# Kernel optimization log

Measured on AMD Instinct MI355X. Metric: run time of the kernel, lower is better.

## Reference

```python
import jax, jax.numpy as jnp
import numpy as np
from jax import lax

# dims (match init_kwargs)
NC, BS, H, W, OC, NT = 4, 16, 64, 64, 12, 32


def _conv(x, w):
    # NHWC 'same' 3x3 conv
    return lax.conv_general_dilated(x, w, (1, 1), 'SAME',
                                    dimension_numbers=('NHWC', 'HWIO', 'NHWC'))


def _convlstm_step(x, h, c, Wx, Wh, b):
    # Keras ConvLSTM2D, single timestep. Gate order i, f, g(c), o; activation=tanh,
    # recurrent_activation=hard_sigmoid.
    z = _conv(x, Wx) + _conv(h, Wh) + b
    i, f, g, o = jnp.split(z, 4, axis=-1)
    i = jax.nn.hard_sigmoid(i)
    f = jax.nn.hard_sigmoid(f)
    o = jax.nn.hard_sigmoid(o)
    c_new = f * c + i * jnp.tanh(g)
    h_new = o * jnp.tanh(c_new)
    return h_new, c_new


def setup_inputs() -> dict:
    key = jax.random.key(0)
    ks = jax.random.split(key, 8)
    sc = lambda k, shp: jax.random.normal(k, shp, jnp.float32) * 0.05
    return {
        'x': jax.random.normal(ks[0], (BS, NT, H, W, OC), jnp.float32),
        'class_ids': jax.random.randint(ks[1], (NT,), 0, NC),
        'Wx_g': sc(ks[2], (3, 3, NC * OC, 4 * OC)),  # general cell input kernel
        'Wh_g': sc(ks[3], (3, 3, OC, 4 * OC)),       # general cell recurrent kernel
        'b_g': jnp.zeros((4 * OC,), jnp.float32),
        'Wx_c': sc(ks[4], (3, 3, 2 * OC, 4 * OC)),   # class cell input kernel
        'Wh_c': sc(ks[5], (3, 3, OC, 4 * OC)),       # class cell recurrent kernel
        'b_c': jnp.zeros((4 * OC,), jnp.float32),
    }


def reference(x, class_ids, Wx_g, Wh_g, b_g, Wx_c, Wh_c, b_c):
    def step(carry, inp):
        class_h, class_c, gen_h, gen_c = carry
        frame, cid = inp
        # general cell reads the whole class-state bank (raw reshape, as in TF source)
        x_gen = jnp.reshape(class_h, (BS, H, W, NC * OC))
        gen_h, gen_c = _convlstm_step(x_gen, gen_h, gen_c, Wx_g, Wh_g, b_g)
        # class cell reads frame + fresh general representation
        aug = jnp.concatenate([frame, gen_h], axis=-1)  # (BS,H,W,2*OC)
        h_new, c_new = _convlstm_step(aug, class_h[cid], class_c[cid], Wx_c, Wh_c, b_c)
        # scatter update into class-indexed state banks
        class_h = class_h.at[cid].set(h_new)
        class_c = class_c.at[cid].set(c_new)
        return (class_h, class_c, gen_h, gen_c), h_new.reshape(BS, -1)

    z = jnp.zeros((NC, BS, H, W, OC), jnp.float32)
    g = jnp.zeros((BS, H, W, OC), jnp.float32)
    xs = (jnp.swapaxes(x, 0, 1), class_ids)  # time-major
    _, outs = lax.scan(step, (z, z, g, g), xs)
    # OuterLayer: sum over time of flattened per-step outputs
    return jnp.sum(outs, axis=0)  # (BS, H*W*OC)
```

## Files before the change

### kernel.cpp

```cpp
#include <hip/hip_runtime.h>
#include <hip/hip_bf16.h>

#define NCLS 4
#define BS   16
#define NT   32
#define OC   12
#define HW   4096
#define PIX  65536
#define STATE 786432
#define BANK  3145728

typedef short bf16x8 __attribute__((ext_vector_type(8)));
typedef float f32x4  __attribute__((ext_vector_type(4)));

__device__ __forceinline__ float hsig(float v){
    return fminf(fmaxf((v + 3.0f) * (1.0f/6.0f), 0.0f), 1.0f);
}
__device__ __forceinline__ short f2bf(float f){
    union { __hip_bfloat16 h; short s; } u;
    u.h = __float2bfloat16(f);
    return u.s;
}

__global__ __launch_bounds__(256) void repack_kernel(
    const float* __restrict__ Wxg, const float* __restrict__ Whg,
    const float* __restrict__ Wxc, const float* __restrict__ Whc,
    bf16x8* __restrict__ wgt)
{
    int id = blockIdx.x * 256 + threadIdx.x;
    if (id >= 6912) return;
    int cell = id / 3456;
    int rem  = id - cell * 3456;
    int tap  = rem / 384;  rem -= tap * 384;
    int kb   = rem / 192;  rem -= kb * 192;
    int nt   = rem / 64;
    int lane = rem - nt * 64;
    int quad = lane >> 4;
    int n    = nt * 16 + (lane & 15);
    union { bf16x8 v; short s[8]; } o;
    #pragma unroll
    for (int j = 0; j < 8; ++j){
        int k = kb * 32 + quad * 8 + j;
        float f = 0.0f;
        if (cell == 0){
            if (k < 48)      f = Wxg[(tap*48 + k)*48 + n];
            else if (k < 60) f = Whg[(tap*12 + (k-48))*48 + n];
        } else {
            if (k < 24)      f = Wxc[(tap*24 + k)*48 + n];
            else if (k < 36) f = Whc[(tap*12 + (k-24))*48 + n];
        }
        o.s[j] = f2bf(f);
    }
    wgt[id] = o.v;
}

#define HALO_SHORTS (4*198*8)

__device__ __forceinline__ int row_swizzle(int bid){
    return ((bid & 7) << 7) | (bid >> 3);
}

__global__ __launch_bounds__(256, 4) void gen_kernel(
    short* __restrict__ bank,
    const short* __restrict__ hin,
    short* __restrict__ hout,
    float* __restrict__ cstate,
    const short* __restrict__ htmp_prev,
    const int* __restrict__ ids, int t,
    const bf16x8* __restrict__ wgt,
    const float* __restrict__ bias)
{
    __shared__ __align__(16) short halo[HALO_SHORTS];
    const int tid = threadIdx.x;
    const int rb  = row_swizzle(blockIdx.x);
    const int p0  = rb << 6;
    const int b   = p0 >> 12;
    const int y   = (p0 >> 6) & 63;

    const int cprev = (t > 0) ? ids[t-1] : -1;
    const bool slotmatch = (cprev >= 0) && ((b >> 2) == cprev);
    const short* bsrc = slotmatch ? htmp_prev : bank;

    const int i = tid;
    const bool active = (i < 198);
    {
        int r  = i / 66, c = i - r * 66;
        int yy = y + r - 1, xx = c - 1;
        bool valid = active & (yy >= 0) & (yy < 64) & (xx >= 0) & (xx < 64);
        int p  = (b << 12) + (yy << 6) + xx;
        int pb = slotmatch ? (p & 16383) : p;
        uint4 bk[6]; uint2 h0, h1, h2;
        #pragma unroll
        for (int q = 0; q < 6; ++q) bk[q] = make_uint4(0u,0u,0u,0u);
        h0 = make_uint2(0u,0u); h1 = h0; h2 = h0;
        if (valid){
            const short* bp = bsrc + pb*48;
            #pragma unroll
            for (int q = 0; q < 6; ++q) bk[q] = *(const uint4*)(bp + q*8);
            h0 = *(const uint2*)(hin + p*12);
            h1 = *(const uint2*)(hin + p*12 + 4);
            h2 = *(const uint2*)(hin + p*12 + 8);
            if (slotmatch && r == 1){
                #pragma unroll
                for (int q = 0; q < 6; ++q)
                    *(uint4*)(bank + p*48 + q*8) = bk[q];
            }
        }
        if (active){
            #pragma unroll
            for (int q = 0; q < 4; ++q)
                *(uint4*)&halo[(q*198 + i)*8] = bk[q];
        }
        __syncthreads();

        const int lane = tid & 63;
        const int w    = tid >> 6;
        const int m    = lane & 15;
        const int quad = lane >> 4;
        const int colbase = 16*w + m;

        f32x4 acc0 = {0.f,0.f,0.f,0.f};
        f32x4 acc1 = acc0, acc2 = acc0;

        #pragma unroll
        for (int ky = 0; ky < 3; ++ky){
            #pragma unroll
            for (int kx = 0; kx < 3; ++kx){
                const int tap = ky*3 + kx;
                const bf16x8 a = *(const bf16x8*)
                    &halo[((quad*198) + ky*66 + colbase + kx)*8];
                const bf16x8* wp = wgt + ((tap*2 + 0)*3)*64 + lane;
                acc0 = __builtin_amdgcn_mfma_f32_16x16x32_bf16(a, wp[0],   acc0, 0,0,0);
                acc1 = __builtin_amdgcn_mfma_f32_16x16x32_bf16(a, wp[64],  acc1, 0,0,0);
                acc2 = __builtin_amdgcn_mfma_f32_16x16x32_bf16(a, wp[128], acc2, 0,0,0);
            }
        }
        __syncthreads();

        if (active){
            *(uint4*)&halo[(0*198 + i)*8] = bk[4];
            *(uint4*)&halo[(1*198 + i)*8] = bk[5];
            union { uint2 u2[2]; uint4 u4; } p2, p3;
            p2.u2[0] = h0; p2.u2[1] = h1;
            p3.u2[0] = h2; p3.u2[1] = make_uint2(0u,0u);
            *(uint4*)&halo[(2*198 + i)*8] = p2.u4;
            *(uint4*)&halo[(3*198 + i)*8] = p3.u4;
        }
        __syncthreads();

        #pragma unroll
        for (int ky = 0; ky < 3; ++ky){
            #pragma unroll
            for (int kx = 0; kx < 3; ++kx){
                const int tap = ky*3 + kx;
                const bf16x8 a = *(const bf16x8*)
                    &halo[((quad*198) + ky*66 + colbase + kx)*8];
                const bf16x8* wp = wgt + ((tap*2 + 1)*3)*64 + lane;
                acc0 = __builtin_amdgcn_mfma_f32_16x16x32_bf16(a, wp[0],   acc0, 0,0,0);
                acc1 = __builtin_amdgcn_mfma_f32_16x16x32_bf16(a, wp[64],  acc1, 0,0,0);
                acc2 = __builtin_amdgcn_mfma_f32_16x16x32_bf16(a, wp[128], acc2, 0,0,0);
            }
        }
        __syncthreads();

        float* zw = ((float*)halo) + w * 768;
        #pragma unroll
        for (int r2 = 0; r2 < 4; ++r2){
            zw[(quad*4 + r2)*48 +      m] = acc0[r2];
            zw[(quad*4 + r2)*48 + 16 + m] = acc1[r2];
            zw[(quad*4 + r2)*48 + 32 + m] = acc2[r2];
        }
        __syncthreads();
        const int pbase = p0 + 16*w;
        #pragma unroll
        for (int s = 0; s < 3; ++s){
            int idx = lane*3 + s;
            int px  = idx / 12;
            int j   = idx - px*12;
            float zi = zw[px*48 +      j] + bias[j];
            float zf = zw[px*48 + 12 + j] + bias[12 + j];
            float zg = zw[px*48 + 24 + j] + bias[24 + j];
            float zo = zw[px*48 + 36 + j] + bias[36 + j];
            int off = pbase*12 + idx;
            float cold = cstate[off];
            float cn = hsig(zf)*cold + hsig(zi)*tanhf(zg);
            cstate[off] = cn;
            hout[off] = f2bf(hsig(zo)*tanhf(cn));
        }
    }
}

__global__ __launch_bounds__(256, 4) void class_kernel(
    const float* __restrict__ xall,
    const int*   __restrict__ ids, int t,
    const short* __restrict__ ghn,
    const short* __restrict__ bank,
    float* __restrict__ class_c,
    const bf16x8* __restrict__ wgt,
    const float* __restrict__ bias,
    short* __restrict__ htmp,
    float* __restrict__ out)
{
    __shared__ __align__(16) short halo[HALO_SHORTS];
    const int tid = threadIdx.x;
    const int rb  = row_swizzle(blockIdx.x);
    const int p0  = rb << 6;
    const int b   = p0 >> 12;
    const int y   = (p0 >> 6) & 63;
    const int cid = ids[t];
    const short* chs   = bank + (size_t)cid * STATE;
    const float* frame = xall + (size_t)(b*NT + t) * (HW*12);

    const int i = tid;
    const bool active = (i < 198);
    {
        int r  = i / 66, c = i - r * 66;
        int yy = y + r - 1, xx = c - 1;
        bool valid = active & (yy >= 0) & (yy < 64) & (xx >= 0) & (xx < 64);
        int pl = (yy << 6) + xx;
        int p  = (b << 12) + pl;
        float4 f0, f1, f2;
        f0 = make_float4(0.f,0.f,0.f,0.f); f1 = f0; f2 = f0;
        uint2 g0, g1, g2, s0, s1, s2;
        g0 = make_uint2(0u,0u); g1 = g0; g2 = g0; s0 = g0; s1 = g0; s2 = g0;
        if (valid){
            f0 = *(const float4*)(frame + pl*12);
            f1 = *(const float4*)(frame + pl*12 + 4);
            f2 = *(const float4*)(frame + pl*12 + 8);
            g0 = *(const uint2*)(ghn + p*12);
            g1 = *(const uint2*)(ghn + p*12 + 4);
            g2 = *(const uint2*)(ghn + p*12 + 8);
            s0 = *(const uint2*)(chs + p*12);
            s1 = *(const uint2*)(chs + p*12 + 4);
            s2 = *(const uint2*)(chs + p*12 + 8);
        }
        if (active){
            union { uint4 u4; uint2 u2[2]; short s[8]; } pk;
            pk.s[0]=f2bf(f0.x); pk.s[1]=f2bf(f0.y); pk.s[2]=f2bf(f0.z); pk.s[3]=f2bf(f0.w);
            pk.s[4]=f2bf(f1.x); pk.s[5]=f2bf(f1.y); pk.s[6]=f2bf(f1.z); pk.s[7]=f2bf(f1.w);
            *(uint4*)&halo[(0*198 + i)*8] = pk.u4;
            pk.s[0]=f2bf(f2.x); pk.s[1]=f2bf(f2.y); pk.s[2]=f2bf(f2.z); pk.s[3]=f2bf(f2.w);
            pk.u2[1] = g0;
            *(uint4*)&halo[(1*198 + i)*8] = pk.u4;
            pk.u2[0] = g1; pk.u2[1] = g2;
            *(uint4*)&halo[(2*198 + i)*8] = pk.u4;
            pk.u2[0] = s0; pk.u2[1] = s1;
            *(uint4*)&halo[(3*198 + i)*8] = pk.u4;
        }
        __syncthreads();

        const int lane = tid & 63;
        const int w    = tid >> 6;
        const int m    = lane & 15;
        const int quad = lane >> 4;
        const int colbase = 16*w + m;

        f32x4 acc0 = {0.f,0.f,0.f,0.f};
        f32x4 acc1 = acc0, acc2 = acc0;

        #pragma unroll
        for (int ky = 0; ky < 3; ++ky){
            #pragma unroll
            for (int kx = 0; kx < 3; ++kx){
                const int tap = ky*3 + kx;
                const bf16x8 a = *(const bf16x8*)
                    &halo[((quad*198) + ky*66 + colbase + kx)*8];
                const bf16x8* wp = wgt + ((tap*2 + 0)*3)*64 + lane;
                acc0 = __builtin_amdgcn_mfma_f32_16x16x32_bf16(a, wp[0],   acc0, 0,0,0);
                acc1 = __builtin_amdgcn_mfma_f32_16x16x32_bf16(a, wp[64],  acc1, 0,0,0);
                acc2 = __builtin_amdgcn_mfma_f32_16x16x32_bf16(a, wp[128], acc2, 0,0,0);
            }
        }
        __syncthreads();

        if (active){
            union { uint4 u4; uint2 u2[2]; } p0k;
            p0k.u2[0] = s2; p0k.u2[1] = make_uint2(0u,0u);
            uint4 z = make_uint4(0u,0u,0u,0u);
            *(uint4*)&halo[(0*198 + i)*8] = p0k.u4;
            *(uint4*)&halo[(1*198 + i)*8] = z;
            *(uint4*)&halo[(2*198 + i)*8] = z;
            *(uint4*)&halo[(3*198 + i)*8] = z;
        }
        __syncthreads();

        #pragma unroll
        for (int ky = 0; ky < 3; ++ky){
            #pragma unroll
            for (int kx = 0; kx < 3; ++kx){
                const int tap = ky*3 + kx;
                const bf16x8 a = *(const bf16x8*)
                    &halo[((quad*198) + ky*66 + colbase + kx)*8];
                const bf16x8* wp = wgt + ((tap*2 + 1)*3)*64 + lane;
                acc0 = __builtin_amdgcn_mfma_f32_16x16x32_bf16(a, wp[0],   acc0, 0,0,0);
                acc1 = __builtin_amdgcn_mfma_f32_16x16x32_bf16(a, wp[64],  acc1, 0,0,0);
                acc2 = __builtin_amdgcn_mfma_f32_16x16x32_bf16(a, wp[128], acc2, 0,0,0);
            }
        }
        __syncthreads();

        float* zw = ((float*)halo) + w * 768;
        #pragma unroll
        for (int r2 = 0; r2 < 4; ++r2){
            zw[(quad*4 + r2)*48 +      m] = acc0[r2];
            zw[(quad*4 + r2)*48 + 16 + m] = acc1[r2];
            zw[(quad*4 + r2)*48 + 32 + m] = acc2[r2];
        }
        __syncthreads();
        float* cc = class_c + (size_t)cid * STATE;
        const int pbase = p0 + 16*w;
        #pragma unroll
        for (int s = 0; s < 3; ++s){
            int idx = lane*3 + s;
            int px  = idx / 12;
            int j   = idx - px*12;
            float zi = zw[px*48 +      j] + bias[j];
            float zf = zw[px*48 + 12 + j] + bias[12 + j];
            float zg = zw[px*48 + 24 + j] + bias[24 + j];
            float zo = zw[px*48 + 36 + j] + bias[36 + j];
            int off = pbase*12 + idx;
            float cold = cc[off];
            float cn = hsig(zf)*cold + hsig(zi)*tanhf(zg);
            cc[off] = cn;
            float h = hsig(zo)*tanhf(cn);
            htmp[off] = f2bf(h);
            out[off] += h;
        }
    }
}

extern "C" void kernel_launch(void* const* d_in, const int* in_sizes, int n_in,
                              void* d_out, int out_size, void* d_ws, size_t ws_size,
                              hipStream_t stream)
{
    (void)in_sizes; (void)n_in; (void)out_size; (void)ws_size;
    const float* x    = (const float*)d_in[0];
    const int*   ids  = (const int*)  d_in[1];
    const float* Wxg  = (const float*)d_in[2];
    const float* Whg  = (const float*)d_in[3];
    const float* bg   = (const float*)d_in[4];
    const float* Wxc  = (const float*)d_in[5];
    const float* Whc  = (const float*)d_in[6];
    const float* bc   = (const float*)d_in[7];
    float* out = (float*)d_out;

    char* base = (char*)d_ws;
    short*  bank    = (short*) (base);
    float*  class_c = (float*) (base + 6291456);
    short*  genh0   = (short*) (base + 18874368);
    short*  genh1   = (short*) (base + 20447232);
    float*  gen_c   = (float*) (base + 22020096);
    short*  htmp0   = (short*) (base + 25165824);
    short*  htmp1   = (short*) (base + 26738688);
    bf16x8* wgt     = (bf16x8*)(base + 28311552);
    const bf16x8* wgt_gen = wgt;
    const bf16x8* wgt_cls = wgt + 3456;

    hipMemsetAsync(bank,    0, (size_t)2*BANK,  stream);
    hipMemsetAsync(class_c, 0, (size_t)4*BANK,  stream);
    hipMemsetAsync(genh0,   0, (size_t)2*STATE, stream);
    hipMemsetAsync(gen_c,   0, (size_t)4*STATE, stream);
    hipMemsetAsync(out,     0, (size_t)4*STATE, stream);

    repack_kernel<<<27, 256, 0, stream>>>(Wxg, Whg, Wxc, Whc, wgt);

    for (int t = 0; t < NT; ++t){
        short* hin       = (t & 1) ? genh1 : genh0;
        short* hnew      = (t & 1) ? genh0 : genh1;
        short* htmp_prev = (t & 1) ? htmp0 : htmp1;
        short* htmp_new  = (t & 1) ? htmp1 : htmp0;
        gen_kernel<<<1024, 256, 0, stream>>>(bank, hin, hnew, gen_c,
                                             htmp_prev, ids, t, wgt_gen, bg);
        class_kernel<<<1024, 256, 0, stream>>>(x, ids, t, hnew, bank, class_c,
                                               wgt_cls, bc, htmp_new, out);
    }
}
```

Measured before the change: 1.065 ms.

## Fuse general and class ConvLSTM cells into one per-step kernel with halo recompute

Merges the two per-timestep kernels into a single step kernel. Each block recomputes the general cell over three rows (its own row plus neighbours) so the class cell's 3x3 conv can read the fresh general hidden state from shared memory without a grid-wide dependency. This halves the launches and removes a global round-trip of the general hidden state. It also pre-converts x to bf16 once, and double-buffers the general cell state so neighbouring blocks read unmodified values. The cost is about three times the general-cell MFMA work per block, plus more shared memory, and occupancy drops to 2 blocks per CU.

```diff
diff --git a/kernel.cpp b/kernel.cpp
--- a/kernel.cpp
+++ b/kernel.cpp
@@ -12,6 +12,7 @@
 
 typedef short bf16x8 __attribute__((ext_vector_type(8)));
 typedef float f32x4  __attribute__((ext_vector_type(4)));
+typedef unsigned long long u64;
 
 __device__ __forceinline__ float hsig(float v){
     return fminf(fmaxf((v + 3.0f) * (1.0f/6.0f), 0.0f), 1.0f);
@@ -54,279 +55,230 @@
     wgt[id] = o.v;
 }
 
-#define HALO_SHORTS (4*198*8)
+__global__ __launch_bounds__(256) void cvt_kernel(
+    const float* __restrict__ x, short* __restrict__ xbf)
+{
+    for (int i = blockIdx.x*256 + threadIdx.x; i < 6291456; i += 2048*256){
+        float4 f = ((const float4*)x)[i];
+        union { u64 q; short s[4]; } pk;
+        pk.s[0]=f2bf(f.x); pk.s[1]=f2bf(f.y); pk.s[2]=f2bf(f.z); pk.s[3]=f2bf(f.w);
+        ((u64*)xbf)[i] = pk.q;
+    }
+}
+
+#define REC 72
 
 __device__ __forceinline__ int row_swizzle(int bid){
     return ((bid & 7) << 7) | (bid >> 3);
 }
 
-__global__ __launch_bounds__(256, 4) void gen_kernel(
+#define MFMA __builtin_amdgcn_mfma_f32_16x16x32_bf16
+
+__global__ __launch_bounds__(256, 2) void step_kernel(
+    const short* __restrict__ xbf,
+    const int*   __restrict__ ids, int t,
     short* __restrict__ bank,
-    const short* __restrict__ hin,
-    short* __restrict__ hout,
-    float* __restrict__ cstate,
-    const short* __restrict__ htmp_prev,
-    const int* __restrict__ ids, int t,
+    const short* __restrict__ hin,  short* __restrict__ hnew,
+    const short* __restrict__ htp,  short* __restrict__ htn,
+    const float* __restrict__ gcs,  float* __restrict__ gcd,
+    float* __restrict__ class_c,
     const bf16x8* __restrict__ wgt,
-    const float* __restrict__ bias)
+    const float* __restrict__ bias_g, const float* __restrict__ bias_c,
+    float* __restrict__ out)
 {
-    __shared__ __align__(16) short halo[HALO_SHORTS];
+    __shared__ __align__(16) short grec[5*66*REC];
+    __shared__ __align__(16) short crec[3*66*REC];
+    __shared__ __align__(8)  short hrow[768];
+
     const int tid = threadIdx.x;
     const int rb  = row_swizzle(blockIdx.x);
     const int p0  = rb << 6;
     const int b   = p0 >> 12;
     const int y   = (p0 >> 6) & 63;
-
+    const int lane = tid & 63, w = tid >> 6, m = lane & 15, quad = lane >> 4;
+    const int colbase = 16*w + m;
+    const int cid   = ids[t];
     const int cprev = (t > 0) ? ids[t-1] : -1;
     const bool slotmatch = (cprev >= 0) && ((b >> 2) == cprev);
-    const short* bsrc = slotmatch ? htmp_prev : bank;
-
-    const int i = tid;
-    const bool active = (i < 198);
+    const bf16x8* wgt_cls = wgt + 3456;
+    const short* xframe = xbf + (size_t)(b*NT + t)*(HW*12);
+    const short* chs = (cid == cprev) ? htp : (bank + (size_t)cid*STATE);
+
     {
-        int r  = i / 66, c = i - r * 66;
-        int yy = y + r - 1, xx = c - 1;
-        bool valid = active & (yy >= 0) & (yy < 64) & (xx >= 0) & (xx < 64);
-        int p  = (b << 12) + (yy << 6) + xx;
-        int pb = slotmatch ? (p & 16383) : p;
-        uint4 bk[6]; uint2 h0, h1, h2;
-        #pragma unroll
-        for (int q = 0; q < 6; ++q) bk[q] = make_uint4(0u,0u,0u,0u);
-        h0 = make_uint2(0u,0u); h1 = h0; h2 = h0;
-        if (valid){
-            const short* bp = bsrc + pb*48;
+        const uint4 z = make_uint4(0u,0u,0u,0u);
+        uint4* g4 = (uint4*)grec;
+        for (int j = tid; j < 2970; j += 256) g4[j] = z;
+        uint4* c4 = (uint4*)crec;
+        for (int j = tid; j < 1782; j += 256) c4[j] = z;
+    }
+    __syncthreads();
+
+    for (int pos = tid; pos < 330; pos += 256){
+        int r = pos/66, c = pos - r*66;
+        int yy = y + r - 2, xx = c - 1;
+        if (yy >= 0 && yy < 64 && xx >= 0 && xx < 64){
+            int p = (b<<12) + (yy<<6) + xx;
+            const short* src = slotmatch ? (htp + (size_t)(p & 16383)*48)
+                                         : (bank + (size_t)p*48);
+            short* dst = &grec[pos*REC];
+            uint4 v[6];
             #pragma unroll
-            for (int q = 0; q < 6; ++q) bk[q] = *(const uint4*)(bp + q*8);
-            h0 = *(const uint2*)(hin + p*12);
-            h1 = *(const uint2*)(hin + p*12 + 4);
-            h2 = *(const uint2*)(hin + p*12 + 8);
-            if (slotmatch && r == 1){
+            for (int q = 0; q < 6; ++q) v[q] = *(const uint4*)(src + q*8);
+            #pragma unroll
+            for (int q = 0; q < 6; ++q) *(uint4*)(dst + q*8) = v[q];
+            *(u64*)(dst+48) = *(const u64*)(hin + (size_t)p*12);
+            *(u64*)(dst+52) = *(const u64*)(hin + (size_t)p*12 + 4);
+            *(u64*)(dst+56) = *(const u64*)(hin + (size_t)p*12 + 8);
+            if (slotmatch && r == 2){
                 #pragma unroll
                 for (int q = 0; q < 6; ++q)
-                    *(uint4*)(bank + p*48 + q*8) = bk[q];
+                    *(uint4*)(bank + (size_t)p*48 + q*8) = v[q];
             }
         }
-        if (active){
-            #pragma unroll
-            for (int q = 0; q < 4; ++q)
-                *(uint4*)&halo[(q*198 + i)*8] = bk[q];
-        }
-        __syncthreads();
-
-        const int lane = tid & 63;
-        const int w    = tid >> 6;
-        const int m    = lane & 15;
-        const int quad = lane >> 4;
-        const int colbase = 16*w + m;
-
-        f32x4 acc0 = {0.f,0.f,0.f,0.f};
-        f32x4 acc1 = acc0, acc2 = acc0;
-
+    }
+    if (tid < 198){
+        int pos = tid;
+        int r = pos/66, c = pos - r*66;
+        int yy = y + r - 1, xx = c - 1;
+        if (yy >= 0 && yy < 64 && xx >= 0 && xx < 64){
+            int p   = (b<<12) + (yy<<6) + xx;
+            int pim = (yy<<6) + xx;
+            short* dst = &crec[pos*REC];
+            *(u64*)(dst+0)  = *(const u64*)(xframe + (size_t)pim*12);
+            *(u64*)(dst+4)  = *(const u64*)(xframe + (size_t)pim*12 + 4);
+            *(u64*)(dst+8)  = *(const u64*)(xframe + (size_t)pim*12 + 8);
+            *(u64*)(dst+24) = *(const u64*)(chs + (size_t)p*12);
+            *(u64*)(dst+28) = *(const u64*)(chs + (size_t)p*12 + 4);
+            *(u64*)(dst+32) = *(const u64*)(chs + (size_t)p*12 + 8);
+        }
+    }
+    __syncthreads();
+
+    f32x4 ga[3][3];
+    #pragma unroll
+    for (int rr = 0; rr < 3; ++rr){
+        #pragma unroll
+        for (int q = 0; q < 3; ++q){
+            f32x4 zz = {0.f,0.f,0.f,0.f};
+            ga[rr][q] = zz;
+        }
+    }
+    #pragma unroll
+    for (int rr = 0; rr < 3; ++rr){
         #pragma unroll
         for (int ky = 0; ky < 3; ++ky){
             #pragma unroll
             for (int kx = 0; kx < 3; ++kx){
                 const int tap = ky*3 + kx;
-                const bf16x8 a = *(const bf16x8*)
-                    &halo[((quad*198) + ky*66 + colbase + kx)*8];
-                const bf16x8* wp = wgt + ((tap*2 + 0)*3)*64 + lane;
-                acc0 = __builtin_amdgcn_mfma_f32_16x16x32_bf16(a, wp[0],   acc0, 0,0,0);
-                acc1 = __builtin_amdgcn_mfma_f32_16x16x32_bf16(a, wp[64],  acc1, 0,0,0);
-                acc2 = __builtin_amdgcn_mfma_f32_16x16x32_bf16(a, wp[128], acc2, 0,0,0);
+                const int rec = ((rr+ky)*66 + colbase + kx)*REC;
+                const bf16x8 a0 = *(const bf16x8*)&grec[rec + quad*8];
+                const bf16x8 a1 = *(const bf16x8*)&grec[rec + 32 + quad*8];
+                const bf16x8* wp0 = wgt + ((tap*2 + 0)*3)*64 + lane;
+                const bf16x8* wp1 = wgt + ((tap*2 + 1)*3)*64 + lane;
+                ga[rr][0] = MFMA(a0, wp0[0],   ga[rr][0], 0,0,0);
+                ga[rr][1] = MFMA(a0, wp0[64],  ga[rr][1], 0,0,0);
+                ga[rr][2] = MFMA(a0, wp0[128], ga[rr][2], 0,0,0);
+                ga[rr][0] = MFMA(a1, wp1[0],   ga[rr][0], 0,0,0);
+                ga[rr][1] = MFMA(a1, wp1[64],  ga[rr][1], 0,0,0);
+                ga[rr][2] = MFMA(a1, wp1[128], ga[rr][2], 0,0,0);
             }
         }
+    }
+    __syncthreads();
+
+    float* zw = ((float*)grec) + w * 768;
+    #pragma unroll
+    for (int rr = 0; rr < 3; ++rr){
+        int oy = y + rr - 1;
+        if (oy < 0 || oy > 63) continue;
+        #pragma unroll
+        for (int r2 = 0; r2 < 4; ++r2){
+            zw[(quad*4 + r2)*48 +      m] = ga[rr][0][r2];
+            zw[(quad*4 + r2)*48 + 16 + m] = ga[rr][1][r2];
+            zw[(quad*4 + r2)*48 + 32 + m] = ga[rr][2][r2];
+        }
         __syncthreads();
-
-        if (active){
-            *(uint4*)&halo[(0*198 + i)*8] = bk[4];
-            *(uint4*)&halo[(1*198 + i)*8] = bk[5];
-            union { uint2 u2[2]; uint4 u4; } p2, p3;
-            p2.u2[0] = h0; p2.u2[1] = h1;
-            p3.u2[0] = h2; p3.u2[1] = make_uint2(0u,0u);
-            *(uint4*)&halo[(2*198 + i)*8] = p2.u4;
-            *(uint4*)&halo[(3*198 + i)*8] = p3.u4;
-        }
-        __syncthreads();
-
-        #pragma unroll
-        for (int ky = 0; ky < 3; ++ky){
-            #pragma unroll
-            for (int kx = 0; kx < 3; ++kx){
-                const int tap = ky*3 + kx;
-                const bf16x8 a = *(const bf16x8*)
-                    &halo[((quad*198) + ky*66 + colbase + kx)*8];
-                const bf16x8* wp = wgt + ((tap*2 + 1)*3)*64 + lane;
-                acc0 = __builtin_amdgcn_mfma_f32_16x16x32_bf16(a, wp[0],   acc0, 0,0,0);
-                acc1 = __builtin_amdgcn_mfma_f32_16x16x32_bf16(a, wp[64],  acc1, 0,0,0);
-                acc2 = __builtin_amdgcn_mfma_f32_16x16x32_bf16(a, wp[128], acc2, 0,0,0);
-            }
-        }
-        __syncthreads();
-
-        float* zw = ((float*)halo) + w * 768;
-        #pragma unroll
-        for (int r2 = 0; r2 < 4; ++r2){
-            zw[(quad*4 + r2)*48 +      m] = acc0[r2];
-            zw[(quad*4 + r2)*48 + 16 + m] = acc1[r2];
-            zw[(quad*4 + r2)*48 + 32 + m] = acc2[r2];
-        }
-        __syncthreads();
-        const int pbase = p0 + 16*w;
+        const int obase = (b<<12) + (oy<<6) + 16*w;
         #pragma unroll
         for (int s = 0; s < 3; ++s){
             int idx = lane*3 + s;
             int px  = idx / 12;
             int j   = idx - px*12;
-            float zi = zw[px*48 +      j] + bias[j];
-            float zf = zw[px*48 + 12 + j] + bias[12 + j];
-            float zg = zw[px*48 + 24 + j] + bias[24 + j];
-            float zo = zw[px*48 + 36 + j] + bias[36 + j];
-            int off = pbase*12 + idx;
-            float cold = cstate[off];
+            float zi = zw[px*48 +      j] + bias_g[j];
+            float zf = zw[px*48 + 12 + j] + bias_g[12 + j];
+            float zg = zw[px*48 + 24 + j] + bias_g[24 + j];
+            float zo = zw[px*48 + 36 + j] + bias_g[36 + j];
+            int off = obase*12 + idx;
+            float cold = gcs[off];
             float cn = hsig(zf)*cold + hsig(zi)*tanhf(zg);
-            cstate[off] = cn;
-            hout[off] = f2bf(hsig(zo)*tanhf(cn));
-        }
-    }
-}
-
-__global__ __launch_bounds__(256, 4) void class_kernel(
-    const float* __restrict__ xall,
-    const int*   __restrict__ ids, int t,
-    const short* __restrict__ ghn,
-    const short* __restrict__ bank,
-    float* __restrict__ class_c,
-    const bf16x8* __restrict__ wgt,
-    const float* __restrict__ bias,
-    short* __restrict__ htmp,
-    float* __restrict__ out)
-{
-    __shared__ __align__(16) short halo[HALO_SHORTS];
-    const int tid = threadIdx.x;
-    const int rb  = row_swizzle(blockIdx.x);
-    const int p0  = rb << 6;
-    const int b   = p0 >> 12;
-    const int y   = (p0 >> 6) & 63;
-    const int cid = ids[t];
-    const short* chs   = bank + (size_t)cid * STATE;
-    const float* frame = xall + (size_t)(b*NT + t) * (HW*12);
-
-    const int i = tid;
-    const bool active = (i < 198);
+            if (rr == 1) gcd[off] = cn;
+            float h = hsig(zo)*tanhf(cn);
+            crec[(rr*66 + 16*w + px + 1)*REC + 12 + j] = f2bf(h);
+            if (rr == 1) hrow[w*192 + idx] = f2bf(h);
+        }
+        __syncthreads();
+    }
+    __syncthreads();
+
+    if (tid < 192)
+        ((u64*)(hnew + (size_t)p0*12))[tid] = ((const u64*)hrow)[tid];
+
+    f32x4 ca[3];
     {
-        int r  = i / 66, c = i - r * 66;
-        int yy = y + r - 1, xx = c - 1;
-        bool valid = active & (yy >= 0) & (yy < 64) & (xx >= 0) & (xx < 64);
-        int pl = (yy << 6) + xx;
-        int p  = (b << 12) + pl;
-        float4 f0, f1, f2;
-        f0 = make_float4(0.f,0.f,0.f,0.f); f1 = f0; f2 = f0;
-        uint2 g0, g1, g2, s0, s1, s2;
-        g0 = make_uint2(0u,0u); g1 = g0; g2 = g0; s0 = g0; s1 = g0; s2 = g0;
-        if (valid){
-            f0 = *(const float4*)(frame + pl*12);
-            f1 = *(const float4*)(frame + pl*12 + 4);
-            f2 = *(const float4*)(frame + pl*12 + 8);
-            g0 = *(const uint2*)(ghn + p*12);
-            g1 = *(const uint2*)(ghn + p*12 + 4);
-            g2 = *(const uint2*)(ghn + p*12 + 8);
-            s0 = *(const uint2*)(chs + p*12);
-            s1 = *(const uint2*)(chs + p*12 + 4);
-            s2 = *(const uint2*)(chs + p*12 + 8);
-        }
-        if (active){
-            union { uint4 u4; uint2 u2[2]; short s[8]; } pk;
-            pk.s[0]=f2bf(f0.x); pk.s[1]=f2bf(f0.y); pk.s[2]=f2bf(f0.z); pk.s[3]=f2bf(f0.w);
-            pk.s[4]=f2bf(f1.x); pk.s[5]=f2bf(f1.y); pk.s[6]=f2bf(f1.z); pk.s[7]=f2bf(f1.w);
-            *(uint4*)&halo[(0*198 + i)*8] = pk.u4;
-            pk.s[0]=f2bf(f2.x); pk.s[1]=f2bf(f2.y); pk.s[2]=f2bf(f2.z); pk.s[3]=f2bf(f2.w);
-            pk.u2[1] = g0;
-            *(uint4*)&halo[(1*198 + i)*8] = pk.u4;
-            pk.u2[0] = g1; pk.u2[1] = g2;
-            *(uint4*)&halo[(2*198 + i)*8] = pk.u4;
-            pk.u2[0] = s0; pk.u2[1] = s1;
-            *(uint4*)&halo[(3*198 + i)*8] = pk.u4;
-        }
-        __syncthreads();
-
-        const int lane = tid & 63;
-        const int w    = tid >> 6;
-        const int m    = lane & 15;
-        const int quad = lane >> 4;
-        const int colbase = 16*w + m;
-
-        f32x4 acc0 = {0.f,0.f,0.f,0.f};
-        f32x4 acc1 = acc0, acc2 = acc0;
-
-        #pragma unroll
-        for (int ky = 0; ky < 3; ++ky){
-            #pragma unroll
-            for (int kx = 0; kx < 3; ++kx){
-                const int tap = ky*3 + kx;
-                const bf16x8 a = *(const bf16x8*)
-                    &halo[((quad*198) + ky*66 + colbase + kx)*8];
-                const bf16x8* wp = wgt + ((tap*2 + 0)*3)*64 + lane;
-                acc0 = __builtin_amdgcn_mfma_f32_16x16x32_bf16(a, wp[0],   acc0, 0,0,0);
-                acc1 = __builtin_amdgcn_mfma_f32_16x16x32_bf16(a, wp[64],  acc1, 0,0,0);
-                acc2 = __builtin_amdgcn_mfma_f32_16x16x32_bf16(a, wp[128], acc2, 0,0,0);
-            }
-        }
-        __syncthreads();
-
-        if (active){
-            union { uint4 u4; uint2 u2[2]; } p0k;
-            p0k.u2[0] = s2; p0k.u2[1] = make_uint2(0u,0u);
-            uint4 z = make_uint4(0u,0u,0u,0u);
-            *(uint4*)&halo[(0*198 + i)*8] = p0k.u4;
-            *(uint4*)&halo[(1*198 + i)*8] = z;
-            *(uint4*)&halo[(2*198 + i)*8] = z;
-            *(uint4*)&halo[(3*198 + i)*8] = z;
-        }
-        __syncthreads();
-
-        #pragma unroll
-        for (int ky = 0; ky < 3; ++ky){
-            #pragma unroll
-            for (int kx = 0; kx < 3; ++kx){
-                const int tap = ky*3 + kx;
-                const bf16x8 a = *(const bf16x8*)
-                    &halo[((quad*198) + ky*66 + colbase + kx)*8];
-                const bf16x8* wp = wgt + ((tap*2 + 1)*3)*64 + lane;
-                acc0 = __builtin_amdgcn_mfma_f32_16x16x32_bf16(a, wp[0],   acc0, 0,0,0);
-                acc1 = __builtin_amdgcn_mfma_f32_16x16x32_bf16(a, wp[64],  acc1, 0,0,0);
-                acc2 = __builtin_amdgcn_mfma_f32_16x16x32_bf16(a, wp[128], acc2, 0,0,0);
-            }
-        }
-        __syncthreads();
-
-        float* zw = ((float*)halo) + w * 768;
-        #pragma unroll
-        for (int r2 = 0; r2 < 4; ++r2){
-            zw[(quad*4 + r2)*48 +      m] = acc0[r2];
-            zw[(quad*4 + r2)*48 + 16 + m] = acc1[r2];
-            zw[(quad*4 + r2)*48 + 32 + m] = acc2[r2];
-        }
-        __syncthreads();
+        f32x4 zz = {0.f,0.f,0.f,0.f};
+        ca[0] = zz; ca[1] = zz; ca[2] = zz;
+    }
+    #pragma unroll
+    for (int ky = 0; ky < 3; ++ky){
+        #pragma unroll
+        for (int kx = 0; kx < 3; ++kx){
+            const int tap = ky*3 + kx;
+            const int rec = (ky*66 + colbase + kx)*REC;
+            const bf16x8 a0 = *(const bf16x8*)&crec[rec + quad*8];
+            const bf16x8 a1 = *(const bf16x8*)&crec[rec + 32 + quad*8];
+            const bf16x8* wp0 = wgt_cls + ((tap*2 + 0)*3)*64 + lane;
+            const bf16x8* wp1 = wgt_cls + ((tap*2 + 1)*3)*64 + lane;
+            ca[0] = MFMA(a0, wp0[0],   ca[0], 0,0,0);
+            ca[1] = MFMA(a0, wp0[64],  ca[1], 0,0,0);
+            ca[2] = MFMA(a0, wp0[128], ca[2], 0,0,0);
+            ca[0] = MFMA(a1, wp1[0],   ca[0], 0,0,0);
+            ca[1] = MFMA(a1, wp1[64],  ca[1], 0,0,0);
+            ca[2] = MFMA(a1, wp1[128], ca[2], 0,0,0);
+        }
+    }
+    __syncthreads();
+
+    #pragma unroll
+    for (int r2 = 0; r2 < 4; ++r2){
+        zw[(quad*4 + r2)*48 +      m] = ca[0][r2];
+        zw[(quad*4 + r2)*48 + 16 + m] = ca[1][r2];
+        zw[(quad*4 + r2)*48 + 32 + m] = ca[2][r2];
+    }
+    __syncthreads();
+    {
         float* cc = class_c + (size_t)cid * STATE;
-        const int pbase = p0 + 16*w;
+        const int obase = p0 + 16*w;
         #pragma unroll
         for (int s = 0; s < 3; ++s){
             int idx = lane*3 + s;
             int px  = idx / 12;
             int j   = idx - px*12;
-            float zi = zw[px*48 +      j] + bias[j];
-            float zf = zw[px*48 + 12 + j] + bias[12 + j];
-            float zg = zw[px*48 + 24 + j] + bias[24 + j];
-            float zo = zw[px*48 + 36 + j] + bias[36 + j];
-            int off = pbase*12 + idx;
+            float zi = zw[px*48 +      j] + bias_c[j];
+            float zf = zw[px*48 + 12 + j] + bias_c[12 + j];
+            float zg = zw[px*48 + 24 + j] + bias_c[24 + j];
+            float zo = zw[px*48 + 36 + j] + bias_c[36 + j];
+            int off = obase*12 + idx;
             float cold = cc[off];
             float cn = hsig(zf)*cold + hsig(zi)*tanhf(zg);
             cc[off] = cn;
             float h = hsig(zo)*tanhf(cn);
-            htmp[off] = f2bf(h);
             out[off] += h;
-        }
-    }
+            hrow[w*192 + idx] = f2bf(h);
+        }
+    }
+    __syncthreads();
+    if (tid < 192)
+        ((u64*)(htn + (size_t)p0*12))[tid] = ((const u64*)hrow)[tid];
 }
 
 extern "C" void kernel_launch(void* const* d_in, const int* in_sizes, int n_in,
@@ -346,32 +298,35 @@
 
     char* base = (char*)d_ws;
     short*  bank    = (short*) (base);
-    float*  class_c = (float*) (base + 6291456);
-    short*  genh0   = (short*) (base + 18874368);
-    short*  genh1   = (short*) (base + 20447232);
-    float*  gen_c   = (float*) (base + 22020096);
-    short*  htmp0   = (short*) (base + 25165824);
-    short*  htmp1   = (short*) (base + 26738688);
-    bf16x8* wgt     = (bf16x8*)(base + 28311552);
-    const bf16x8* wgt_gen = wgt;
-    const bf16x8* wgt_cls = wgt + 3456;
-
-    hipMemsetAsync(bank,    0, (size_t)2*BANK,  stream);
-    hipMemsetAsync(class_c, 0, (size_t)4*BANK,  stream);
-    hipMemsetAsync(genh0,   0, (size_t)2*STATE, stream);
-    hipMemsetAsync(gen_c,   0, (size_t)4*STATE, stream);
-    hipMemsetAsync(out,     0, (size_t)4*STATE, stream);
+    short*  genh0   = (short*) (base + 6291456);
+    short*  genh1   = (short*) (base + 7864320);
+    short*  htmp0   = (short*) (base + 9437184);
+    short*  htmp1   = (short*) (base + 11010048);
+    float*  gen_cA  = (float*) (base + 12582912);
+    float*  gen_cB  = (float*) (base + 15728640);
+    float*  class_c = (float*) (base + 18874368);
+    bf16x8* wgt     = (bf16x8*)(base + 31457280);
+    short*  xbf     = (short*) (base + 31567872);
+
+    hipMemsetAsync(bank,    0, 6291456,  stream);
+    hipMemsetAsync(genh0,   0, 1572864,  stream);
+    hipMemsetAsync(gen_cA,  0, 3145728,  stream);
+    hipMemsetAsync(class_c, 0, 12582912, stream);
+    hipMemsetAsync(out,     0, 3145728,  stream);
 
     repack_kernel<<<27, 256, 0, stream>>>(Wxg, Whg, Wxc, Whc, wgt);
+    cvt_kernel<<<2048, 256, 0, stream>>>(x, xbf);
 
     for (int t = 0; t < NT; ++t){
-        short* hin       = (t & 1) ? genh1 : genh0;
-        short* hnew      = (t & 1) ? genh0 : genh1;
-        short* htmp_prev = (t & 1) ? htmp0 : htmp1;
-        short* htmp_new  = (t & 1) ? htmp1 : htmp0;
-        gen_kernel<<<1024, 256, 0, stream>>>(bank, hin, hnew, gen_c,
-                                             htmp_prev, ids, t, wgt_gen, bg);
-        class_kernel<<<1024, 256, 0, stream>>>(x, ids, t, hnew, bank, class_c,
-                                               wgt_cls, bc, htmp_new, out);
-    }
-}
+        short* hin = (t & 1) ? genh1 : genh0;
+        short* hnw = (t & 1) ? genh0 : genh1;
+        short* htp = (t & 1) ? htmp0 : htmp1;
+        short* htn = (t & 1) ? htmp1 : htmp0;
+        float* gcs = (t & 1) ? gen_cB : gen_cA;
+        float* gcd = (t & 1) ? gen_cA : gen_cB;
+        step_kernel<<<1024, 256, 0, stream>>>(xbf, ids, t, bank,
+                                              hin, hnw, htp, htn,
+                                              gcs, gcd, class_c,
+                                              wgt, bg, bc, out);
+    }
+}
```

After: 1.444 ms. 35.6% more time.
